# Optimization experiments

Hardware: AMD Instinct MI355X
Metric: run time of the kernel (lower is better)

Reference implementation:

```python
import jax, jax.numpy as jnp
import numpy as np

N = 100000
E = 1600000
IN_DIM = 128
OUT_DIM = 128
EDGE_DIM = 4
LN_EPS = 1e-5


def setup_inputs() -> dict:
    key = jax.random.key(0)
    ks = jax.random.split(key, 12)
    s_in = 1.0 / np.sqrt(IN_DIM)
    s_ed = 1.0 / np.sqrt(EDGE_DIM)
    s_out = 1.0 / np.sqrt(OUT_DIM)
    s_cat = 1.0 / np.sqrt(IN_DIM + OUT_DIM)
    return {
        "x": jax.random.normal(ks[0], (N, IN_DIM), jnp.float32),
        "edge_index": jax.random.randint(ks[1], (2, E), 0, N, jnp.int32),
        "edge_attr": jax.random.normal(ks[2], (E, EDGE_DIM), jnp.float32),
        # agg_mlp: Linear(in_dim, out_dim)
        "agg_W": jax.random.uniform(ks[3], (IN_DIM, OUT_DIM), jnp.float32, -s_in, s_in),
        "agg_b": jnp.zeros((OUT_DIM,), jnp.float32),
        # edge_mlp: Linear(edge_dim, out_dim) -> SiLU -> Linear(out_dim, 1) -> Sigmoid
        "edge_W1": jax.random.uniform(ks[4], (EDGE_DIM, OUT_DIM), jnp.float32, -s_ed, s_ed),
        "edge_b1": jnp.zeros((OUT_DIM,), jnp.float32),
        "edge_W2": jax.random.uniform(ks[5], (OUT_DIM, 1), jnp.float32, -s_out, s_out),
        "edge_b2": jnp.zeros((1,), jnp.float32),
        # update_mlp: Linear(in+out, out) -> SiLU -> Linear(out, out)
        "upd_W1": jax.random.uniform(ks[6], (IN_DIM + OUT_DIM, OUT_DIM), jnp.float32, -s_cat, s_cat),
        "upd_b1": jnp.zeros((OUT_DIM,), jnp.float32),
        "upd_W2": jax.random.uniform(ks[7], (OUT_DIM, OUT_DIM), jnp.float32, -s_out, s_out),
        "upd_b2": jnp.zeros((OUT_DIM,), jnp.float32),
        # LayerNorm(out_dim)
        "ln_g": jnp.ones((OUT_DIM,), jnp.float32),
        "ln_b": jnp.zeros((OUT_DIM,), jnp.float32),
        # residual: Linear(in_dim, out_dim, bias=False)
        "res_W": jax.random.uniform(ks[8], (IN_DIM, OUT_DIM), jnp.float32, -s_in, s_in),
    }


def reference(x, edge_index, edge_attr, agg_W, agg_b, edge_W1, edge_b1,
              edge_W2, edge_b2, upd_W1, upd_b1, upd_W2, upd_b2,
              ln_g, ln_b, res_W):
    n = x.shape[0]
    src, dst = edge_index[0], edge_index[1]
    # edge gate: (E, 1)
    e_h = jax.nn.silu(edge_attr @ edge_W1 + edge_b1)
    e_w = jax.nn.sigmoid(e_h @ edge_W2 + edge_b2)
    # gather -> gated message: (E, out_dim)
    x_agg = jax.nn.silu(x[src] @ agg_W + agg_b) * e_w
    # scatter-add mean aggregation
    out = jax.ops.segment_sum(x_agg, dst, num_segments=n)
    cnt = jax.ops.segment_sum(jnp.ones((dst.shape[0],), x.dtype), dst, num_segments=n)
    out = out / jnp.maximum(cnt, 1.0)[:, None]
    # update MLP on concat(x, aggregated)
    h = jnp.concatenate([x, out], axis=-1)
    h = jax.nn.silu(h @ upd_W1 + upd_b1) @ upd_W2 + upd_b2
    # residual + layernorm (dropout is identity in eval mode)
    h = h + x @ res_W
    mu = jnp.mean(h, axis=-1, keepdims=True)
    var = jnp.mean(jnp.square(h - mu), axis=-1, keepdims=True)
    h = (h - mu) * jax.lax.rsqrt(var + LN_EPS) * ln_g + ln_b
    return h
```

## Files before the change

### kernel.cpp

```cpp
#include <hip/hip_runtime.h>
#include <math.h>

#define N_NODES 100000
#define N_EDGES 1600000
#define LN_EPS 1e-5f

#define B_SHIFT 4
#define B_NODES 16
#define N_BUCKETS 6250
#define SEG_CAP 448

typedef __attribute__((ext_vector_type(8))) short short8;
typedef __attribute__((ext_vector_type(4))) float f32x4;
#define MFMA16(a, b, c) __builtin_amdgcn_mfma_f32_16x16x32_bf16(a, b, c, 0, 0, 0)

#define LOG2E 1.442695040888963f

#if __has_builtin(__builtin_amdgcn_exp2f) && __has_builtin(__builtin_amdgcn_rcpf)
__device__ __forceinline__ float sigmoidf_(float v) {
    return __builtin_amdgcn_rcpf(1.0f + __builtin_amdgcn_exp2f(-LOG2E * v));
}
#else
__device__ __forceinline__ float sigmoidf_(float v) { return 1.0f / (1.0f + __expf(-v)); }
#endif
__device__ __forceinline__ float siluf_(float v) { return v * sigmoidf_(v); }

__device__ __forceinline__ unsigned short f2bf_(float f) {
    unsigned int u = __float_as_uint(f);
    unsigned int rounded = u + 0x7FFF + ((u >> 16) & 1);
    return (unsigned short)(rounded >> 16);
}

__global__ __launch_bounds__(256) void kw(const float* __restrict__ W1,
                                          const float* __restrict__ W2,
                                          const float* __restrict__ resW,
                                          const float* __restrict__ aggW,
                                          unsigned short* __restrict__ w1t,
                                          unsigned short* __restrict__ w2t,
                                          unsigned short* __restrict__ rest,
                                          unsigned short* __restrict__ aggt) {
    const int idx = blockIdx.x * 256 + threadIdx.x;
    if (idx < 32768) {
        const int n = idx >> 8, k = idx & 255;
        w1t[idx] = f2bf_(W1[k * 128 + n]);
    } else if (idx < 49152) {
        const int i = idx - 32768, n = i >> 7, k = i & 127;
        w2t[i] = f2bf_(W2[k * 128 + n]);
    } else if (idx < 65536) {
        const int i = idx - 49152, n = i >> 7, k = i & 127;
        rest[i] = f2bf_(resW[k * 128 + n]);
    } else {
        const int i = idx - 65536, n = i >> 7, k = i & 127;
        aggt[i] = f2bf_(aggW[k * 128 + n]);
    }
}

__global__ __launch_bounds__(256) void k1_y(const float* __restrict__ x,
                                            const unsigned short* __restrict__ aggt,
                                            const float* __restrict__ b,
                                            unsigned short* __restrict__ y16) {
    __shared__ unsigned short A1[32 * 136];
    __shared__ unsigned short O[32 * 136];
    const int t = threadIdx.x;
    const int n0 = blockIdx.x * 32;
    const float4* x4 = (const float4*)x;

#pragma unroll
    for (int r = 0; r < 4; ++r) {
        const int idx = t + r * 256;
        const int node = idx >> 5, c4 = idx & 31;
        const float4 v = x4[(n0 + node) * 32 + c4];
        ushort4 p;
        p.x = f2bf_(v.x); p.y = f2bf_(v.y); p.z = f2bf_(v.z); p.w = f2bf_(v.w);
        *(ushort4*)&A1[node * 136 + c4 * 4] = p;
    }
    __syncthreads();

    const int w = t >> 6, lane = t & 63, nq = lane & 15, quad = lane >> 4;
    f32x4 c[2][2] = {};
#pragma unroll
    for (int ks = 0; ks < 4; ++ks) {
        const int k0 = ks * 32 + quad * 8;
        const short8 a0 = *(const short8*)&A1[(nq)*136 + k0];
        const short8 a1 = *(const short8*)&A1[(16 + nq) * 136 + k0];
        const short8 b0 = *(const short8*)&aggt[(w * 32 + nq) * 128 + k0];
        const short8 b1 = *(const short8*)&aggt[(w * 32 + 16 + nq) * 128 + k0];
        c[0][0] = MFMA16(a0, b0, c[0][0]);
        c[0][1] = MFMA16(a0, b1, c[0][1]);
        c[1][0] = MFMA16(a1, b0, c[1][0]);
        c[1][1] = MFMA16(a1, b1, c[1][1]);
    }
    const float bc0 = b[w * 32 + nq], bc1 = b[w * 32 + 16 + nq];
#pragma unroll
    for (int mt = 0; mt < 2; ++mt)
#pragma unroll
        for (int r = 0; r < 4; ++r) {
            const int row = mt * 16 + quad * 4 + r;
            O[row * 136 + w * 32 + nq] = f2bf_(siluf_(c[mt][0][r] + bc0));
            O[row * 136 + w * 32 + 16 + nq] = f2bf_(siluf_(c[mt][1][r] + bc1));
        }
    __syncthreads();

#pragma unroll
    for (int r = 0; r < 2; ++r) {
        const int idx = t + r * 256;
        const int row = idx >> 4, c8 = idx & 15;
        const short8 v = *(const short8*)&O[row * 136 + c8 * 8];
        *(short8*)&y16[(n0 + row) * 128 + c8 * 8] = v;
    }
}

__global__ __launch_bounds__(256) void p3i(int* __restrict__ bcursor) {
    const int n = blockIdx.x * 256 + threadIdx.x;
    if (n < N_BUCKETS) bcursor[n] = n * SEG_CAP;
}

__global__ __launch_bounds__(128) void p3g(const float* __restrict__ attr,
                                           const float* __restrict__ W1,
                                           const float* __restrict__ b1,
                                           const float* __restrict__ W2,
                                           const float* __restrict__ b2,
                                           const int* __restrict__ src,
                                           const int* __restrict__ dst,
                                           int* __restrict__ bcursor,
                                           uint2* __restrict__ brec) {
    __shared__ float4 W1s[128];
    __shared__ float4 W2s[32];
    __shared__ float4 b1s[32];
    const int t = threadIdx.x;
    W1s[t] = ((const float4*)W1)[t];
    if (t < 32) {
        W2s[t] = ((const float4*)W2)[t];
        b1s[t] = ((const float4*)b1)[t];
    }
    __syncthreads();

    const int e0 = blockIdx.x * 256 + t;
    const int e1 = e0 + 128;
    const float4 a0 = ((const float4*)attr)[e0];
    const float4 a1 = ((const float4*)attr)[e1];
    const int s0 = src[e0], s1 = src[e1];
    const int d0 = dst[e0], d1 = dst[e1];
    float acc0 = 0.f, acc1 = 0.f;
#pragma unroll 8
    for (int j4 = 0; j4 < 32; ++j4) {
        const float4 r0 = W1s[j4];
        const float4 r1 = W1s[32 + j4];
        const float4 r2 = W1s[64 + j4];
        const float4 r3 = W1s[96 + j4];
        const float4 bb = b1s[j4];
        const float4 w2v = W2s[j4];
        float hx = fmaf(a0.x, r0.x, fmaf(a0.y, r1.x, fmaf(a0.z, r2.x, fmaf(a0.w, r3.x, bb.x))));
        float hy = fmaf(a0.x, r0.y, fmaf(a0.y, r1.y, fmaf(a0.z, r2.y, fmaf(a0.w, r3.y, bb.y))));
        float hz = fmaf(a0.x, r0.z, fmaf(a0.y, r1.z, fmaf(a0.z, r2.z, fmaf(a0.w, r3.z, bb.z))));
        float hw = fmaf(a0.x, r0.w, fmaf(a0.y, r1.w, fmaf(a0.z, r2.w, fmaf(a0.w, r3.w, bb.w))));
        float gx = fmaf(a1.x, r0.x, fmaf(a1.y, r1.x, fmaf(a1.z, r2.x, fmaf(a1.w, r3.x, bb.x))));
        float gy = fmaf(a1.x, r0.y, fmaf(a1.y, r1.y, fmaf(a1.z, r2.y, fmaf(a1.w, r3.y, bb.y))));
        float gz = fmaf(a1.x, r0.z, fmaf(a1.y, r1.z, fmaf(a1.z, r2.z, fmaf(a1.w, r3.z, bb.z))));
        float gw = fmaf(a1.x, r0.w, fmaf(a1.y, r1.w, fmaf(a1.z, r2.w, fmaf(a1.w, r3.w, bb.w))));
        acc0 = fmaf(siluf_(hx), w2v.x, acc0);
        acc1 = fmaf(siluf_(gx), w2v.x, acc1);
        acc0 = fmaf(siluf_(hy), w2v.y, acc0);
        acc1 = fmaf(siluf_(gy), w2v.y, acc1);
        acc0 = fmaf(siluf_(hz), w2v.z, acc0);
        acc1 = fmaf(siluf_(gz), w2v.z, acc1);
        acc0 = fmaf(siluf_(hw), w2v.w, acc0);
        acc1 = fmaf(siluf_(gw), w2v.w, acc1);
    }
    const float b2c = b2[0];
    const float ew0 = sigmoidf_(acc0 + b2c);
    const float ew1 = sigmoidf_(acc1 + b2c);
    const int bk0 = d0 >> B_SHIFT;
    const int slot0 = atomicAdd(&bcursor[bk0], 1);
    if (slot0 < (bk0 + 1) * SEG_CAP)
        brec[slot0] = make_uint2((unsigned)s0 | ((unsigned)(d0 & (B_NODES - 1)) << 27),
                                 __float_as_uint(ew0));
    const int bk1 = d1 >> B_SHIFT;
    const int slot1 = atomicAdd(&bcursor[bk1], 1);
    if (slot1 < (bk1 + 1) * SEG_CAP)
        brec[slot1] = make_uint2((unsigned)s1 | ((unsigned)(d1 & (B_NODES - 1)) << 27),
                                 __float_as_uint(ew1));
}

__global__ __launch_bounds__(256) void pB(const unsigned short* __restrict__ y16,
                                          const int* __restrict__ bcursor,
                                          const uint2* __restrict__ brec,
                                          float* __restrict__ agg) {
    __shared__ uint2 raw[SEG_CAP];
    __shared__ uint2 srec[SEG_CAP];
    __shared__ int hist[B_NODES];
    __shared__ int nstart[B_NODES];
    __shared__ int ncur[B_NODES];

    const int t = threadIdx.x;
    const int b = blockIdx.x;
    const int base = b * SEG_CAP;
    int c = bcursor[b] - base;
    if (c > SEG_CAP) c = SEG_CAP;

    if (t < B_NODES) hist[t] = 0;
    __syncthreads();

    for (int i = t; i < c; i += 256) {
        const uint2 r = brec[base + i];
        raw[i] = r;
        atomicAdd(&hist[r.x >> 27], 1);
    }
    __syncthreads();

    if (t == 0) {
        int acc = 0;
#pragma unroll
        for (int d = 0; d < B_NODES; ++d) {
            nstart[d] = acc;
            ncur[d] = acc;
            acc += hist[d];
        }
    }
    __syncthreads();

    for (int i = t; i < c; i += 256) {
        const uint2 r = raw[i];
        const int slot = atomicAdd(&ncur[r.x >> 27], 1);
        srec[slot] = r;
    }
    __syncthreads();

    const int w = t >> 6, lane = t & 63;
    const unsigned int* y32 = (const unsigned int*)y16;
#pragma unroll
    for (int rep = 0; rep < 4; ++rep) {
        const int d = w + rep * 4;
        const int st = nstart[d];
        const int cd = hist[d];
        const int end = st + cd;
        float ax0 = 0.f, ay0 = 0.f, ax1 = 0.f, ay1 = 0.f;
        float ax2 = 0.f, ay2 = 0.f, ax3 = 0.f, ay3 = 0.f;
        int p = st;
        for (; p + 8 <= end; p += 8) {
            const uint2 r0 = srec[p];
            const uint2 r1 = srec[p + 1];
            const uint2 r2 = srec[p + 2];
            const uint2 r3 = srec[p + 3];
            const uint2 r4 = srec[p + 4];
            const uint2 r5 = srec[p + 5];
            const uint2 r6 = srec[p + 6];
            const uint2 r7 = srec[p + 7];
            const unsigned int u0 = y32[(r0.x & 0x7FFFFFFu) * 64 + lane];
            const unsigned int u1 = y32[(r1.x & 0x7FFFFFFu) * 64 + lane];
            const unsigned int u2 = y32[(r2.x & 0x7FFFFFFu) * 64 + lane];
            const unsigned int u3 = y32[(r3.x & 0x7FFFFFFu) * 64 + lane];
            const unsigned int u4 = y32[(r4.x & 0x7FFFFFFu) * 64 + lane];
            const unsigned int u5 = y32[(r5.x & 0x7FFFFFFu) * 64 + lane];
            const unsigned int u6 = y32[(r6.x & 0x7FFFFFFu) * 64 + lane];
            const unsigned int u7 = y32[(r7.x & 0x7FFFFFFu) * 64 + lane];
            const float w0 = __uint_as_float(r0.y);
            const float w1 = __uint_as_float(r1.y);
            const float w2 = __uint_as_float(r2.y);
            const float w3 = __uint_as_float(r3.y);
            const float w4 = __uint_as_float(r4.y);
            const float w5 = __uint_as_float(r5.y);
            const float w6 = __uint_as_float(r6.y);
            const float w7 = __uint_as_float(r7.y);
            ax0 = fmaf(__uint_as_float(u0 << 16), w0, ax0);
            ay0 = fmaf(__uint_as_float(u0 & 0xFFFF0000u), w0, ay0);
            ax1 = fmaf(__uint_as_float(u1 << 16), w1, ax1);
            ay1 = fmaf(__uint_as_float(u1 & 0xFFFF0000u), w1, ay1);
            ax2 = fmaf(__uint_as_float(u2 << 16), w2, ax2);
            ay2 = fmaf(__uint_as_float(u2 & 0xFFFF0000u), w2, ay2);
            ax3 = fmaf(__uint_as_float(u3 << 16), w3, ax3);
            ay3 = fmaf(__uint_as_float(u3 & 0xFFFF0000u), w3, ay3);
            ax0 = fmaf(__uint_as_float(u4 << 16), w4, ax0);
            ay0 = fmaf(__uint_as_float(u4 & 0xFFFF0000u), w4, ay0);
            ax1 = fmaf(__uint_as_float(u5 << 16), w5, ax1);
            ay1 = fmaf(__uint_as_float(u5 & 0xFFFF0000u), w5, ay1);
            ax2 = fmaf(__uint_as_float(u6 << 16), w6, ax2);
            ay2 = fmaf(__uint_as_float(u6 & 0xFFFF0000u), w6, ay2);
            ax3 = fmaf(__uint_as_float(u7 << 16), w7, ax3);
            ay3 = fmaf(__uint_as_float(u7 & 0xFFFF0000u), w7, ay3);
        }
        for (; p + 4 <= end; p += 4) {
            const uint2 r0 = srec[p];
            const uint2 r1 = srec[p + 1];
            const uint2 r2 = srec[p + 2];
            const uint2 r3 = srec[p + 3];
            const unsigned int u0 = y32[(r0.x & 0x7FFFFFFu) * 64 + lane];
            const unsigned int u1 = y32[(r1.x & 0x7FFFFFFu) * 64 + lane];
            const unsigned int u2 = y32[(r2.x & 0x7FFFFFFu) * 64 + lane];
            const unsigned int u3 = y32[(r3.x & 0x7FFFFFFu) * 64 + lane];
            const float w0 = __uint_as_float(r0.y);
            const float w1 = __uint_as_float(r1.y);
            const float w2 = __uint_as_float(r2.y);
            const float w3 = __uint_as_float(r3.y);
            ax0 = fmaf(__uint_as_float(u0 << 16), w0, ax0);
            ay0 = fmaf(__uint_as_float(u0 & 0xFFFF0000u), w0, ay0);
            ax1 = fmaf(__uint_as_float(u1 << 16), w1, ax1);
            ay1 = fmaf(__uint_as_float(u1 & 0xFFFF0000u), w1, ay1);
            ax2 = fmaf(__uint_as_float(u2 << 16), w2, ax2);
            ay2 = fmaf(__uint_as_float(u2 & 0xFFFF0000u), w2, ay2);
            ax3 = fmaf(__uint_as_float(u3 << 16), w3, ax3);
            ay3 = fmaf(__uint_as_float(u3 & 0xFFFF0000u), w3, ay3);
        }
        for (; p < end; ++p) {
            const uint2 r0 = srec[p];
            const unsigned int u0 = y32[(r0.x & 0x7FFFFFFu) * 64 + lane];
            const float w0 = __uint_as_float(r0.y);
            ax0 = fmaf(__uint_as_float(u0 << 16), w0, ax0);
            ay0 = fmaf(__uint_as_float(u0 & 0xFFFF0000u), w0, ay0);
        }
        const float accx = (ax0 + ax1) + (ax2 + ax3);
        const float accy = (ay0 + ay1) + (ay2 + ay3);
        const float inv = 1.0f / fmaxf((float)cd, 1.0f);
        const int n = b * B_NODES + d;
        ((float2*)agg)[n * 64 + lane] = make_float2(accx * inv, accy * inv);
    }
}

__global__ __launch_bounds__(256) void k4_update(const float* __restrict__ x,
                                                 const float* agg,
                                                 const unsigned short* __restrict__ w1t,
                                                 const float* __restrict__ b1,
                                                 const unsigned short* __restrict__ w2t,
                                                 const float* __restrict__ b2,
                                                 const float* __restrict__ lng,
                                                 const float* __restrict__ lnb,
                                                 const unsigned short* __restrict__ rest,
                                                 float* out) {
    __shared__ unsigned short A1[32 * 264];
    __shared__ unsigned short A2[32 * 136];
    __shared__ float red_s[4][32];
    __shared__ float red_q[4][32];
    __shared__ float ln_mu[32];
    __shared__ float ln_rs[32];

    const int t = threadIdx.x;
    const int n0 = blockIdx.x * 32;
    const float4* x4 = (const float4*)x;
    const float4* agg4 = (const float4*)agg;

#pragma unroll
    for (int r = 0; r < 4; ++r) {
        const int idx = t + r * 256;
        const int node = idx >> 5, c4 = idx & 31;
        const float4 vx = x4[(n0 + node) * 32 + c4];
        const float4 va = agg4[(n0 + node) * 32 + c4];
        ushort4 px, pa;
        px.x = f2bf_(vx.x); px.y = f2bf_(vx.y); px.z = f2bf_(vx.z); px.w = f2bf_(vx.w);
        pa.x = f2bf_(va.x); pa.y = f2bf_(va.y); pa.z = f2bf_(va.z); pa.w = f2bf_(va.w);
        *(ushort4*)&A1[node * 264 + c4 * 4] = px;
        *(ushort4*)&A1[node * 264 + 128 + c4 * 4] = pa;
    }
    __syncthreads();

    const int w = t >> 6, lane = t & 63, nq = lane & 15, quad = lane >> 4;

    f32x4 c1[2][2] = {};
#pragma unroll
    for (int ks = 0; ks < 8; ++ks) {
        const int k0 = ks * 32 + quad * 8;
        const short8 a0 = *(const short8*)&A1[(nq)*264 + k0];
        const short8 a1 = *(const short8*)&A1[(16 + nq) * 264 + k0];
        const short8 b0 = *(const short8*)&w1t[(w * 32 + nq) * 256 + k0];
        const short8 b1f = *(const short8*)&w1t[(w * 32 + 16 + nq) * 256 + k0];
        c1[0][0] = MFMA16(a0, b0, c1[0][0]);
        c1[0][1] = MFMA16(a0, b1f, c1[0][1]);
        c1[1][0] = MFMA16(a1, b0, c1[1][0]);
        c1[1][1] = MFMA16(a1, b1f, c1[1][1]);
    }
    const float b1c0 = b1[w * 32 + nq], b1c1 = b1[w * 32 + 16 + nq];
#pragma unroll
    for (int mt = 0; mt < 2; ++mt)
#pragma unroll
        for (int r = 0; r < 4; ++r) {
            const int row = mt * 16 + quad * 4 + r;
            A2[row * 136 + w * 32 + nq] = f2bf_(siluf_(c1[mt][0][r] + b1c0));
            A2[row * 136 + w * 32 + 16 + nq] = f2bf_(siluf_(c1[mt][1][r] + b1c1));
        }
    __syncthreads();

    f32x4 c2[2][2] = {};
#pragma unroll
    for (int ks = 0; ks < 4; ++ks) {
        const int k0 = ks * 32 + quad * 8;
        const short8 a0 = *(const short8*)&A2[(nq)*136 + k0];
        const short8 a1 = *(const short8*)&A2[(16 + nq) * 136 + k0];
        const short8 b0 = *(const short8*)&w2t[(w * 32 + nq) * 128 + k0];
        const short8 b1f = *(const short8*)&w2t[(w * 32 + 16 + nq) * 128 + k0];
        c2[0][0] = MFMA16(a0, b0, c2[0][0]);
        c2[0][1] = MFMA16(a0, b1f, c2[0][1]);
        c2[1][0] = MFMA16(a1, b0, c2[1][0]);
        c2[1][1] = MFMA16(a1, b1f, c2[1][1]);
    }
#pragma unroll
    for (int ks = 0; ks < 4; ++ks) {
        const int k0 = ks * 32 + quad * 8;
        const short8 a0 = *(const short8*)&A1[(nq)*264 + k0];
        const short8 a1 = *(const short8*)&A1[(16 + nq) * 264 + k0];
        const short8 b0 = *(const short8*)&rest[(w * 32 + nq) * 128 + k0];
        const short8 b1f = *(const short8*)&rest[(w * 32 + 16 + nq) * 128 + k0];
        c2[0][0] = MFMA16(a0, b0, c2[0][0]);
        c2[0][1] = MFMA16(a0, b1f, c2[0][1]);
        c2[1][0] = MFMA16(a1, b0, c2[1][0]);
        c2[1][1] = MFMA16(a1, b1f, c2[1][1]);
    }

    const float b2c0 = b2[w * 32 + nq], b2c1 = b2[w * 32 + 16 + nq];
    float vals[2][2][4];
#pragma unroll
    for (int mt = 0; mt < 2; ++mt)
#pragma unroll
        for (int r = 0; r < 4; ++r) {
            vals[mt][0][r] = c2[mt][0][r] + b2c0;
            vals[mt][1][r] = c2[mt][1][r] + b2c1;
        }
#pragma unroll
    for (int mt = 0; mt < 2; ++mt)
#pragma unroll
        for (int r = 0; r < 4; ++r) {
            float s = vals[mt][0][r] + vals[mt][1][r];
            float q = vals[mt][0][r] * vals[mt][0][r] + vals[mt][1][r] * vals[mt][1][r];
#pragma unroll
            for (int off = 1; off <= 8; off <<= 1) {
                s += __shfl_xor(s, off, 64);
                q += __shfl_xor(q, off, 64);
            }
            if (nq == 0) {
                const int row = mt * 16 + quad * 4 + r;
                red_s[w][row] = s;
                red_q[w][row] = q;
            }
        }
    __syncthreads();
    if (t < 32) {
        const float ts = red_s[0][t] + red_s[1][t] + red_s[2][t] + red_s[3][t];
        const float tq = red_q[0][t] + red_q[1][t] + red_q[2][t] + red_q[3][t];
        const float mu = ts * (1.0f / 128.0f);
        const float var = fmaxf(tq * (1.0f / 128.0f) - mu * mu, 0.f);
        ln_mu[t] = mu;
        ln_rs[t] = rsqrtf(var + LN_EPS);
    }
    __syncthreads();

    const float g0 = lng[w * 32 + nq], g1 = lng[w * 32 + 16 + nq];
    const float lb0 = lnb[w * 32 + nq], lb1 = lnb[w * 32 + 16 + nq];
#pragma unroll
    for (int mt = 0; mt < 2; ++mt)
#pragma unroll
        for (int r = 0; r < 4; ++r) {
            const int row = mt * 16 + quad * 4 + r;
            const float mu = ln_mu[row], rs = ln_rs[row];
            out[(n0 + row) * 128 + w * 32 + nq] = (vals[mt][0][r] - mu) * rs * g0 + lb0;
            out[(n0 + row) * 128 + w * 32 + 16 + nq] = (vals[mt][1][r] - mu) * rs * g1 + lb1;
        }
}

extern "C" void kernel_launch(void* const* d_in, const int* in_sizes, int n_in,
                              void* d_out, int out_size, void* d_ws, size_t ws_size,
                              hipStream_t stream) {
    const float* x = (const float*)d_in[0];
    const int* ei = (const int*)d_in[1];
    const float* eattr = (const float*)d_in[2];
    const float* aggW = (const float*)d_in[3];
    const float* aggb = (const float*)d_in[4];
    const float* eW1 = (const float*)d_in[5];
    const float* eb1 = (const float*)d_in[6];
    const float* eW2 = (const float*)d_in[7];
    const float* eb2 = (const float*)d_in[8];
    const float* uW1 = (const float*)d_in[9];
    const float* ub1 = (const float*)d_in[10];
    const float* uW2 = (const float*)d_in[11];
    const float* ub2 = (const float*)d_in[12];
    const float* lng = (const float*)d_in[13];
    const float* lnb = (const float*)d_in[14];
    const float* resW = (const float*)d_in[15];
    float* out = (float*)d_out;

    char* ws = (char*)d_ws;
    unsigned short* y16 = (unsigned short*)(ws + 0);
    uint2* brec = (uint2*)(ws + 25600000);
    int* bcursor = (int*)(ws + 48000000);
    unsigned short* w1t = (unsigned short*)(ws + 48025008);
    unsigned short* w2t = (unsigned short*)(ws + 48090544);
    unsigned short* rest = (unsigned short*)(ws + 48123312);
    unsigned short* aggt = (unsigned short*)(ws + 48156080);
    float* agg = out;

    const int* src = ei;
    const int* dst = ei + N_EDGES;

    kw<<<320, 256, 0, stream>>>(uW1, uW2, resW, aggW, w1t, w2t, rest, aggt);
    k1_y<<<N_NODES / 32, 256, 0, stream>>>(x, aggt, aggb, y16);
    p3i<<<(N_BUCKETS + 255) / 256, 256, 0, stream>>>(bcursor);
    p3g<<<N_EDGES / 256, 128, 0, stream>>>(eattr, eW1, eb1, eW2, eb2,
                                           src, dst, bcursor, brec);
    pB<<<N_BUCKETS, 256, 0, stream>>>(y16, bcursor, brec, agg);
    k4_update<<<N_NODES / 32, 256, 0, stream>>>(x, agg, w1t, ub1, w2t, ub2, lng, lnb, rest, out);
}
```

Measured before the change: 365.6 us.

## Replace per-bucket LDS sort with shared-memory atomic accumulation; fold cursor init into weight kernel

Result: slower. 1.346 ms (+268.2%).

```diff
diff --git a/kernel.cpp b/kernel.cpp
--- a/kernel.cpp
+++ b/kernel.cpp
@@ -38,7 +38,8 @@
                                           unsigned short* __restrict__ w1t,
                                           unsigned short* __restrict__ w2t,
                                           unsigned short* __restrict__ rest,
-                                          unsigned short* __restrict__ aggt) {
+                                          unsigned short* __restrict__ aggt,
+                                          int* __restrict__ bcursor) {
     const int idx = blockIdx.x * 256 + threadIdx.x;
     if (idx < 32768) {
         const int n = idx >> 8, k = idx & 255;
@@ -49,9 +50,12 @@
     } else if (idx < 65536) {
         const int i = idx - 49152, n = i >> 7, k = i & 127;
         rest[i] = f2bf_(resW[k * 128 + n]);
-    } else {
+    } else if (idx < 81920) {
         const int i = idx - 65536, n = i >> 7, k = i & 127;
         aggt[i] = f2bf_(aggW[k * 128 + n]);
+    } else if (idx < 81920 + N_BUCKETS) {
+        const int n = idx - 81920;
+        bcursor[n] = n * SEG_CAP;
     }
 }
 
@@ -108,11 +112,6 @@
         const short8 v = *(const short8*)&O[row * 136 + c8 * 8];
         *(short8*)&y16[(n0 + row) * 128 + c8 * 8] = v;
     }
-}
-
-__global__ __launch_bounds__(256) void p3i(int* __restrict__ bcursor) {
-    const int n = blockIdx.x * 256 + threadIdx.x;
-    if (n < N_BUCKETS) bcursor[n] = n * SEG_CAP;
 }
 
 __global__ __launch_bounds__(128) void p3g(const float* __restrict__ attr,
@@ -186,11 +185,9 @@
                                           const int* __restrict__ bcursor,
                                           const uint2* __restrict__ brec,
                                           float* __restrict__ agg) {
-    __shared__ uint2 raw[SEG_CAP];
-    __shared__ uint2 srec[SEG_CAP];
+    __shared__ float accx[B_NODES][64];
+    __shared__ float accy[B_NODES][64];
     __shared__ int hist[B_NODES];
-    __shared__ int nstart[B_NODES];
-    __shared__ int ncur[B_NODES];
 
     const int t = threadIdx.x;
     const int b = blockIdx.x;
@@ -199,120 +196,78 @@
     if (c > SEG_CAP) c = SEG_CAP;
 
     if (t < B_NODES) hist[t] = 0;
+    for (int i = t; i < B_NODES * 64; i += 256) {
+        ((float*)accx)[i] = 0.f;
+        ((float*)accy)[i] = 0.f;
+    }
     __syncthreads();
 
     for (int i = t; i < c; i += 256) {
-        const uint2 r = brec[base + i];
-        raw[i] = r;
-        atomicAdd(&hist[r.x >> 27], 1);
-    }
-    __syncthreads();
-
-    if (t == 0) {
-        int acc = 0;
-#pragma unroll
-        for (int d = 0; d < B_NODES; ++d) {
-            nstart[d] = acc;
-            ncur[d] = acc;
-            acc += hist[d];
-        }
-    }
-    __syncthreads();
-
-    for (int i = t; i < c; i += 256) {
-        const uint2 r = raw[i];
-        const int slot = atomicAdd(&ncur[r.x >> 27], 1);
-        srec[slot] = r;
-    }
-    __syncthreads();
+        atomicAdd(&hist[brec[base + i].x >> 27], 1);
+    }
 
     const int w = t >> 6, lane = t & 63;
     const unsigned int* y32 = (const unsigned int*)y16;
-#pragma unroll
-    for (int rep = 0; rep < 4; ++rep) {
-        const int d = w + rep * 4;
-        const int st = nstart[d];
-        const int cd = hist[d];
-        const int end = st + cd;
-        float ax0 = 0.f, ay0 = 0.f, ax1 = 0.f, ay1 = 0.f;
-        float ax2 = 0.f, ay2 = 0.f, ax3 = 0.f, ay3 = 0.f;
-        int p = st;
-        for (; p + 8 <= end; p += 8) {
-            const uint2 r0 = srec[p];
-            const uint2 r1 = srec[p + 1];
-            const uint2 r2 = srec[p + 2];
-            const uint2 r3 = srec[p + 3];
-            const uint2 r4 = srec[p + 4];
-            const uint2 r5 = srec[p + 5];
-            const uint2 r6 = srec[p + 6];
-            const uint2 r7 = srec[p + 7];
-            const unsigned int u0 = y32[(r0.x & 0x7FFFFFFu) * 64 + lane];
-            const unsigned int u1 = y32[(r1.x & 0x7FFFFFFu) * 64 + lane];
-            const unsigned int u2 = y32[(r2.x & 0x7FFFFFFu) * 64 + lane];
-            const unsigned int u3 = y32[(r3.x & 0x7FFFFFFu) * 64 + lane];
-            const unsigned int u4 = y32[(r4.x & 0x7FFFFFFu) * 64 + lane];
-            const unsigned int u5 = y32[(r5.x & 0x7FFFFFFu) * 64 + lane];
-            const unsigned int u6 = y32[(r6.x & 0x7FFFFFFu) * 64 + lane];
-            const unsigned int u7 = y32[(r7.x & 0x7FFFFFFu) * 64 + lane];
-            const float w0 = __uint_as_float(r0.y);
-            const float w1 = __uint_as_float(r1.y);
-            const float w2 = __uint_as_float(r2.y);
-            const float w3 = __uint_as_float(r3.y);
-            const float w4 = __uint_as_float(r4.y);
-            const float w5 = __uint_as_float(r5.y);
-            const float w6 = __uint_as_float(r6.y);
-            const float w7 = __uint_as_float(r7.y);
-            ax0 = fmaf(__uint_as_float(u0 << 16), w0, ax0);
-            ay0 = fmaf(__uint_as_float(u0 & 0xFFFF0000u), w0, ay0);
-            ax1 = fmaf(__uint_as_float(u1 << 16), w1, ax1);
-            ay1 = fmaf(__uint_as_float(u1 & 0xFFFF0000u), w1, ay1);
-            ax2 = fmaf(__uint_as_float(u2 << 16), w2, ax2);
-            ay2 = fmaf(__uint_as_float(u2 & 0xFFFF0000u), w2, ay2);
-            ax3 = fmaf(__uint_as_float(u3 << 16), w3, ax3);
-            ay3 = fmaf(__uint_as_float(u3 & 0xFFFF0000u), w3, ay3);
-            ax0 = fmaf(__uint_as_float(u4 << 16), w4, ax0);
-            ay0 = fmaf(__uint_as_float(u4 & 0xFFFF0000u), w4, ay0);
-            ax1 = fmaf(__uint_as_float(u5 << 16), w5, ax1);
-            ay1 = fmaf(__uint_as_float(u5 & 0xFFFF0000u), w5, ay1);
-            ax2 = fmaf(__uint_as_float(u6 << 16), w6, ax2);
-            ay2 = fmaf(__uint_as_float(u6 & 0xFFFF0000u), w6, ay2);
-            ax3 = fmaf(__uint_as_float(u7 << 16), w7, ax3);
-            ay3 = fmaf(__uint_as_float(u7 & 0xFFFF0000u), w7, ay3);
-        }
-        for (; p + 4 <= end; p += 4) {
-            const uint2 r0 = srec[p];
-            const uint2 r1 = srec[p + 1];
-            const uint2 r2 = srec[p + 2];
-            const uint2 r3 = srec[p + 3];
-            const unsigned int u0 = y32[(r0.x & 0x7FFFFFFu) * 64 + lane];
-            const unsigned int u1 = y32[(r1.x & 0x7FFFFFFu) * 64 + lane];
-            const unsigned int u2 = y32[(r2.x & 0x7FFFFFFu) * 64 + lane];
-            const unsigned int u3 = y32[(r3.x & 0x7FFFFFFu) * 64 + lane];
-            const float w0 = __uint_as_float(r0.y);
-            const float w1 = __uint_as_float(r1.y);
-            const float w2 = __uint_as_float(r2.y);
-            const float w3 = __uint_as_float(r3.y);
-            ax0 = fmaf(__uint_as_float(u0 << 16), w0, ax0);
-            ay0 = fmaf(__uint_as_float(u0 & 0xFFFF0000u), w0, ay0);
-            ax1 = fmaf(__uint_as_float(u1 << 16), w1, ax1);
-            ay1 = fmaf(__uint_as_float(u1 & 0xFFFF0000u), w1, ay1);
-            ax2 = fmaf(__uint_as_float(u2 << 16), w2, ax2);
-            ay2 = fmaf(__uint_as_float(u2 & 0xFFFF0000u), w2, ay2);
-            ax3 = fmaf(__uint_as_float(u3 << 16), w3, ax3);
-            ay3 = fmaf(__uint_as_float(u3 & 0xFFFF0000u), w3, ay3);
-        }
-        for (; p < end; ++p) {
-            const uint2 r0 = srec[p];
-            const unsigned int u0 = y32[(r0.x & 0x7FFFFFFu) * 64 + lane];
-            const float w0 = __uint_as_float(r0.y);
-            ax0 = fmaf(__uint_as_float(u0 << 16), w0, ax0);
-            ay0 = fmaf(__uint_as_float(u0 & 0xFFFF0000u), w0, ay0);
-        }
-        const float accx = (ax0 + ax1) + (ax2 + ax3);
-        const float accy = (ay0 + ay1) + (ay2 + ay3);
-        const float inv = 1.0f / fmaxf((float)cd, 1.0f);
-        const int n = b * B_NODES + d;
-        ((float2*)agg)[n * 64 + lane] = make_float2(accx * inv, accy * inv);
+    const int cq = (c + 3) >> 2;
+    int p = w * cq;
+    int pend = (w + 1) * cq;
+    if (pend > c) pend = c;
+    for (; p + 8 <= pend; p += 8) {
+        const uint2 r0 = brec[base + p];
+        const uint2 r1 = brec[base + p + 1];
+        const uint2 r2 = brec[base + p + 2];
+        const uint2 r3 = brec[base + p + 3];
+        const uint2 r4 = brec[base + p + 4];
+        const uint2 r5 = brec[base + p + 5];
+        const uint2 r6 = brec[base + p + 6];
+        const uint2 r7 = brec[base + p + 7];
+        const unsigned int u0 = y32[(r0.x & 0x7FFFFFFu) * 64 + lane];
+        const unsigned int u1 = y32[(r1.x & 0x7FFFFFFu) * 64 + lane];
+        const unsigned int u2 = y32[(r2.x & 0x7FFFFFFu) * 64 + lane];
+        const unsigned int u3 = y32[(r3.x & 0x7FFFFFFu) * 64 + lane];
+        const unsigned int u4 = y32[(r4.x & 0x7FFFFFFu) * 64 + lane];
+        const unsigned int u5 = y32[(r5.x & 0x7FFFFFFu) * 64 + lane];
+        const unsigned int u6 = y32[(r6.x & 0x7FFFFFFu) * 64 + lane];
+        const unsigned int u7 = y32[(r7.x & 0x7FFFFFFu) * 64 + lane];
+        const float w0 = __uint_as_float(r0.y);
+        const float w1 = __uint_as_float(r1.y);
+        const float w2 = __uint_as_float(r2.y);
+        const float w3 = __uint_as_float(r3.y);
+        const float w4 = __uint_as_float(r4.y);
+        const float w5 = __uint_as_float(r5.y);
+        const float w6 = __uint_as_float(r6.y);
+        const float w7 = __uint_as_float(r7.y);
+        atomicAdd(&accx[r0.x >> 27][lane], __uint_as_float(u0 << 16) * w0);
+        atomicAdd(&accy[r0.x >> 27][lane], __uint_as_float(u0 & 0xFFFF0000u) * w0);
+        atomicAdd(&accx[r1.x >> 27][lane], __uint_as_float(u1 << 16) * w1);
+        atomicAdd(&accy[r1.x >> 27][lane], __uint_as_float(u1 & 0xFFFF0000u) * w1);
+        atomicAdd(&accx[r2.x >> 27][lane], __uint_as_float(u2 << 16) * w2);
+        atomicAdd(&accy[r2.x >> 27][lane], __uint_as_float(u2 & 0xFFFF0000u) * w2);
+        atomicAdd(&accx[r3.x >> 27][lane], __uint_as_float(u3 << 16) * w3);
+        atomicAdd(&accy[r3.x >> 27][lane], __uint_as_float(u3 & 0xFFFF0000u) * w3);
+        atomicAdd(&accx[r4.x >> 27][lane], __uint_as_float(u4 << 16) * w4);
+        atomicAdd(&accy[r4.x >> 27][lane], __uint_as_float(u4 & 0xFFFF0000u) * w4);
+        atomicAdd(&accx[r5.x >> 27][lane], __uint_as_float(u5 << 16) * w5);
+        atomicAdd(&accy[r5.x >> 27][lane], __uint_as_float(u5 & 0xFFFF0000u) * w5);
+        atomicAdd(&accx[r6.x >> 27][lane], __uint_as_float(u6 << 16) * w6);
+        atomicAdd(&accy[r6.x >> 27][lane], __uint_as_float(u6 & 0xFFFF0000u) * w6);
+        atomicAdd(&accx[r7.x >> 27][lane], __uint_as_float(u7 << 16) * w7);
+        atomicAdd(&accy[r7.x >> 27][lane], __uint_as_float(u7 & 0xFFFF0000u) * w7);
+    }
+    for (; p < pend; ++p) {
+        const uint2 r0 = brec[base + p];
+        const unsigned int u0 = y32[(r0.x & 0x7FFFFFFu) * 64 + lane];
+        const float w0 = __uint_as_float(r0.y);
+        atomicAdd(&accx[r0.x >> 27][lane], __uint_as_float(u0 << 16) * w0);
+        atomicAdd(&accy[r0.x >> 27][lane], __uint_as_float(u0 & 0xFFFF0000u) * w0);
+    }
+    __syncthreads();
+
+    for (int i = t; i < B_NODES * 64; i += 256) {
+        const int node = i >> 6, l2 = i & 63;
+        const float inv = 1.0f / fmaxf((float)hist[node], 1.0f);
+        ((float2*)agg)[(b * B_NODES + node) * 64 + l2] =
+            make_float2(accx[node][l2] * inv, accy[node][l2] * inv);
     }
 }
 
@@ -488,9 +443,8 @@
     const int* src = ei;
     const int* dst = ei + N_EDGES;
 
-    kw<<<320, 256, 0, stream>>>(uW1, uW2, resW, aggW, w1t, w2t, rest, aggt);
+    kw<<<346, 256, 0, stream>>>(uW1, uW2, resW, aggW, w1t, w2t, rest, aggt, bcursor);
     k1_y<<<N_NODES / 32, 256, 0, stream>>>(x, aggt, aggb, y16);
-    p3i<<<(N_BUCKETS + 255) / 256, 256, 0, stream>>>(bcursor);
     p3g<<<N_EDGES / 256, 128, 0, stream>>>(eattr, eW1, eb1, eW2, eb2,
                                            src, dst, bcursor, brec);
     pB<<<N_BUCKETS, 256, 0, stream>>>(y16, bcursor, brec, agg);
```
